# Kernel tuning notes

Hardware: AMD Instinct MI355X
Metric: run time of the kernel (lower is better)

## Reference

```python
import jax, jax.numpy as jnp
import numpy as np

B = 65536
FEAT = 64
NUM_CONT = 2
NUM_DISC = FEAT - NUM_CONT  # 62
D = 16                      # embedding_size
H1, H2 = 256, 128           # hidden_dims
DNN_IN = FEAT * D           # 1024


def setup_inputs() -> dict:
    key = jax.random.key(0)
    ks = jax.random.split(key, 12)
    # x: first NUM_DISC cols are binary category ids (stored as float), last NUM_CONT are 'continuous'
    x = jax.random.randint(ks[0], (B, FEAT), 0, 2).astype(jnp.float32)
    s = 0.05
    return {
        "x": x,
        # 62 embedding tables of shape (2, D), stacked: [NUM_DISC, 2, D]
        "emb_tables": jax.random.normal(ks[1], (NUM_DISC, 2, D), jnp.float32) * s,
        "Wc": jax.random.normal(ks[2], (NUM_CONT * D, NUM_CONT), jnp.float32) * s,  # cont_linear
        "bc": jnp.zeros((NUM_CONT * D,), jnp.float32),
        "Wf": jax.random.normal(ks[3], (1, FEAT), jnp.float32) * s,                 # fm_linear
        "bf": jnp.zeros((1,), jnp.float32),
        "W1": jax.random.normal(ks[4], (H1, DNN_IN), jnp.float32) * s,
        "b1": jnp.zeros((H1,), jnp.float32),
        "W2": jax.random.normal(ks[5], (H2, H1), jnp.float32) * s,
        "b2": jnp.zeros((H2,), jnp.float32),
    }


def reference(x, emb_tables, Wc, bc, Wf, bf, W1, b1, W2, b2):
    # --- embeddings ---
    disc_idx = x[:, :NUM_DISC].astype(jnp.int32)                     # [B, 62]
    # per-feature table gather: emb_tables[f, idx[b,f]] -> [B, 62, D]
    disc_embeds = emb_tables[jnp.arange(NUM_DISC)[None, :], disc_idx]
    cont = x[:, NUM_DISC:]                                           # [B, 2]
    cont_embeds = (cont @ Wc.T + bc).reshape(-1, NUM_CONT, D)        # [B, 2, D]
    all_embeds = jnp.concatenate([disc_embeds, cont_embeds], axis=1) # [B, 64, D]

    # --- FM first order ---
    fm_first = x @ Wf.T + bf                                         # [B, 1]

    # --- FM second order: sum_{i<j} <e_i, e_j> = 0.5 * ((sum_i e_i)^2 - sum_i e_i^2) summed over D
    sum_e = jnp.sum(all_embeds, axis=1)                              # [B, D]
    sum_sq = jnp.sum(all_embeds * all_embeds, axis=(1, 2))           # [B]
    fm_second = 0.5 * (jnp.sum(sum_e * sum_e, axis=1) - sum_sq)      # [B]
    fm_second = fm_second[:, None]                                   # [B, 1]

    # --- DNN ---
    h = all_embeds.reshape(x.shape[0], -1)                           # [B, 1024]
    h = jax.nn.relu(h @ W1.T + b1)                                   # [B, 256]
    h = jax.nn.relu(h @ W2.T + b2)                                   # [B, 128]

    return jnp.concatenate([fm_first + fm_second, h], axis=1)        # [B, 129]
```

## Files before the change

### kernel.cpp

```cpp
#include <hip/hip_runtime.h>
#include <hip/hip_bf16.h>


#define NROWS   65536
#define NFEAT   64
#define NDISC   62
#define DIM     16
#define K1      1024
#define H1N     256
#define H2N     128
#define OUTC    129

using f32x4  = __attribute__((ext_vector_type(4))) float;
using bf16x8 = __attribute__((ext_vector_type(8))) short;

__device__ __forceinline__ unsigned short f2bf(float f) {
    unsigned u = __builtin_bit_cast(unsigned, f);
    u = (u + 0x7FFFu + ((u >> 16) & 1u)) >> 16;
    return (unsigned short)u;
}

__device__ __forceinline__ void async16(const void* g, void* l) {
    __builtin_amdgcn_global_load_lds(
        (const __attribute__((address_space(1))) void*)g,
        (__attribute__((address_space(3))) void*)l, 16, 0, 0);
}

__global__ __launch_bounds__(256) void convert_w(const float* __restrict__ W1,
                                                 const float* __restrict__ W2,
                                                 unsigned short* __restrict__ W1b,
                                                 unsigned short* __restrict__ W2b) {
    int i = blockIdx.x * 256 + threadIdx.x;
    if (i < H1N * K1) W1b[i] = f2bf(W1[i]);
    if (i < H2N * H1N) W2b[i] = f2bf(W2[i]);
}

__global__ __launch_bounds__(256) void fm_kernel(const float* __restrict__ x,
                                                 const float* __restrict__ tbl,
                                                 const float* __restrict__ Wc,
                                                 const float* __restrict__ bc,
                                                 const float* __restrict__ Wf,
                                                 const float* __restrict__ bfp,
                                                 float* __restrict__ out) {
    __shared__ float tblL[NDISC * 2 * DIM];
    __shared__ float WcL[64];
    __shared__ float bcL[32];
    __shared__ float WfL[64];
    const int t = threadIdx.x, l = t & 63, w = t >> 6;
    const int d = l & 15;
    for (int i = t; i < NDISC * 2 * DIM; i += 256) tblL[i] = tbl[i];
    if (t < 64) WcL[t] = Wc[t];
    else if (t < 96) bcL[t - 64] = bc[t - 64];
    else if (t < 160) WfL[t - 96] = Wf[t - 96];
    __syncthreads();
    const float bf0 = bfp[0];

    const int waveId = blockIdx.x * 4 + w;
    #pragma unroll
    for (int it = 0; it < 2; ++it) {
        const int grp = waveId + it * 8192;
        const int row = grp * 4 + (l >> 4);
        const float4 v = *(const float4*)(x + (size_t)row * NFEAT + d * 4);

        unsigned long long m =
            ((unsigned long long)((int)v.x & 1)) |
            ((unsigned long long)((int)v.y & 1) << 1) |
            ((unsigned long long)((int)v.z & 1) << 2) |
            ((unsigned long long)((int)v.w & 1) << 3);
        m <<= (d * 4);
        m |= __shfl_xor(m, 1); m |= __shfl_xor(m, 2);
        m |= __shfl_xor(m, 4); m |= __shfl_xor(m, 8);
        const float c0 = __shfl(v.z, l | 15);
        const float c1 = __shfl(v.w, l | 15);

        float fp = v.x * WfL[4 * d] + v.y * WfL[4 * d + 1] +
                   v.z * WfL[4 * d + 2] + v.w * WfL[4 * d + 3];

        float se = 0.f, ssq = 0.f;
        #pragma unroll
        for (int f = 0; f < NDISC; ++f) {
            const int bit = (int)((m >> f) & 1ULL);
            const float e = tblL[(f * 2 + bit) * DIM + d];
            se += e; ssq += e * e;
        }
        {
            const float e62 = bcL[d]      + c0 * WcL[2 * d]        + c1 * WcL[2 * d + 1];
            const float e63 = bcL[16 + d] + c0 * WcL[2 * (16 + d)] + c1 * WcL[2 * (16 + d) + 1];
            se += e62 + e63; ssq += e62 * e62 + e63 * e63;
        }

        float u = se * se - ssq;
        u  += __shfl_xor(u, 1);  u  += __shfl_xor(u, 2);
        u  += __shfl_xor(u, 4);  u  += __shfl_xor(u, 8);
        fp += __shfl_xor(fp, 1); fp += __shfl_xor(fp, 2);
        fp += __shfl_xor(fp, 4); fp += __shfl_xor(fp, 8);
        if (d == 0) out[(size_t)row * OUTC] = fp + bf0 + 0.5f * u;
    }
}

__global__ __launch_bounds__(512, 4) void gemm_fused(
        const float* __restrict__ x,
        const float* __restrict__ tbl,
        const float* __restrict__ Wc,
        const float* __restrict__ bc,
        const unsigned short* __restrict__ W1b,
        const float* __restrict__ b1,
        const unsigned short* __restrict__ W2b,
        const float* __restrict__ b2,
        float* __restrict__ out) {
    __shared__ __align__(16) char smem[65536];
    unsigned short* ldsA  = (unsigned short*)(smem);
    unsigned short* ldsB  = (unsigned short*)(smem + 16384);
    unsigned char*  xb    = (unsigned char*)(smem + 49152);
    float*          contf = (float*)(smem + 57344);
    unsigned short* tblLb = (unsigned short*)(smem + 58368);
    float*          WcL   = (float*)(smem + 62336);
    float*          bcL   = (float*)(smem + 62592);
    unsigned short* H1t   = (unsigned short*)(smem);

    const int t  = threadIdx.x;
    const int l  = t & 63;
    const int w  = t >> 6;
    const int wr = w >> 2;
    const int wc = w & 3;
    const int m0 = blockIdx.x * 128;

    for (int i = t; i < NDISC * 2 * DIM; i += 512) tblLb[i] = f2bf(tbl[i]);
    if (t < 64) WcL[t] = Wc[t];
    if (t >= 64 && t < 96) bcL[t - 64] = bc[t - 64];

    {
        const int row = t >> 2, cbase = (t & 3) * 16;
        const float4* xp = (const float4*)(x + (size_t)(m0 + row) * NFEAT + cbase);
        #pragma unroll
        for (int q = 0; q < 4; ++q) {
            float4 v = xp[q];
            unsigned pk = ((unsigned)(int)v.x) | ((unsigned)(int)v.y << 8) |
                          ((unsigned)(int)v.z << 16) | ((unsigned)(int)v.w << 24);
            *(unsigned*)&xb[row * 64 + cbase + q * 4] = pk;
            if (cbase + q * 4 == 60) {
                contf[row * 2]     = v.z;
                contf[row * 2 + 1] = v.w;
            }
        }
    }
    __syncthreads();

    f32x4 acc[4][4] = {};

    for (int ks = 0; ks < 16; ++ks) {
        const int k0 = ks * 64;
        const int f0 = ks * 4;

        #pragma unroll
        for (int p = 0; p < 2; ++p) {
            const int chunk = p * 512 + t;
            const int row = chunk >> 3;
            const int cc  = chunk & 7;
            const int fl  = cc >> 1;
            const int d0  = (cc & 1) * 8;
            const int f   = f0 + fl;
            bf16x8 pk;
            if (f < NDISC) {
                const int bit = xb[row * 64 + f] & 1;
                pk = *(const bf16x8*)&tblLb[(f * 2 + bit) * DIM + d0];
            } else {
                const float c0v = contf[row * 2], c1v = contf[row * 2 + 1];
                const int j0 = (f - NDISC) * 16 + d0;
                #pragma unroll
                for (int dd = 0; dd < 8; ++dd) {
                    const int j = j0 + dd;
                    pk[dd] = (short)f2bf(bcL[j] + c0v * WcL[2 * j] + c1v * WcL[2 * j + 1]);
                }
            }
            *(bf16x8*)&ldsA[row * 64 + (cc ^ (row & 7)) * 8] = pk;
        }

        {
            unsigned short* dstbase = ldsB + w * 512;
            #pragma unroll
            for (int p = 0; p < 4; ++p) {
                const int chunk = p * 512 + t;
                const int row = chunk >> 3;
                const int cc  = chunk & 7;
                const int ccs = cc ^ (row & 7);
                async16(W1b + (size_t)row * K1 + k0 + ccs * 8, dstbase + p * 4096);
            }
        }
        __syncthreads();

        #pragma unroll
        for (int sub = 0; sub < 2; ++sub) {
            const int s = sub * 4 + (l >> 4);
            bf16x8 af[4], bfr[4];
            #pragma unroll
            for (int i = 0; i < 4; ++i) {
                const int ra = wr * 64 + i * 16 + (l & 15);
                af[i] = *(const bf16x8*)&ldsA[ra * 64 + (s ^ (ra & 7)) * 8];
            }
            #pragma unroll
            for (int j = 0; j < 4; ++j) {
                const int rb = wc * 64 + j * 16 + (l & 15);
                bfr[j] = *(const bf16x8*)&ldsB[rb * 64 + (s ^ (rb & 7)) * 8];
            }
            #pragma unroll
            for (int i = 0; i < 4; ++i)
                #pragma unroll
                for (int j = 0; j < 4; ++j)
                    acc[i][j] = __builtin_amdgcn_mfma_f32_16x16x32_bf16(af[i], bfr[j], acc[i][j], 0, 0, 0);
        }
        __syncthreads();
    }

    #pragma unroll
    for (int i = 0; i < 4; ++i) {
        const int rloc0 = wr * 64 + i * 16 + (l >> 4) * 4;
        #pragma unroll
        for (int j = 0; j < 4; ++j) {
            const int col  = wc * 64 + j * 16 + (l & 15);
            const int slot = col >> 3, cin = col & 7;
            const float bias = b1[col];
            #pragma unroll
            for (int r = 0; r < 4; ++r) {
                const int row = rloc0 + r;
                float v = acc[i][j][r] + bias;
                v = v > 0.f ? v : 0.f;
                H1t[row * 256 + (slot ^ (row & 7)) * 8 + cin] = f2bf(v);
            }
        }
    }
    __syncthreads();

    f32x4 acc2[4][2] = {};
    #pragma unroll
    for (int kk = 0; kk < 8; ++kk) {
        bf16x8 bfr2[2];
        #pragma unroll
        for (int j2 = 0; j2 < 2; ++j2) {
            const int nrow = wc * 32 + j2 * 16 + (l & 15);
            bfr2[j2] = *(const bf16x8*)(W2b + (size_t)nrow * H1N + kk * 32 + (l >> 4) * 8);
        }
        const int slot = kk * 4 + (l >> 4);
        #pragma unroll
        for (int i2 = 0; i2 < 4; ++i2) {
            const int ra = wr * 64 + i2 * 16 + (l & 15);
            const bf16x8 af2 = *(const bf16x8*)&H1t[ra * 256 + (slot ^ (ra & 7)) * 8];
            #pragma unroll
            for (int j2 = 0; j2 < 2; ++j2)
                acc2[i2][j2] = __builtin_amdgcn_mfma_f32_16x16x32_bf16(af2, bfr2[j2], acc2[i2][j2], 0, 0, 0);
        }
    }

    #pragma unroll
    for (int i2 = 0; i2 < 4; ++i2) {
        const int rbase = m0 + wr * 64 + i2 * 16 + (l >> 4) * 4;
        #pragma unroll
        for (int j2 = 0; j2 < 2; ++j2) {
            const int n = wc * 32 + j2 * 16 + (l & 15);
            const float bias = b2[n];
            #pragma unroll
            for (int r = 0; r < 4; ++r) {
                float v = acc2[i2][j2][r] + bias;
                v = v > 0.f ? v : 0.f;
                out[(size_t)(rbase + r) * OUTC + 1 + n] = v;
            }
        }
    }
}

extern "C" void kernel_launch(void* const* d_in, const int* in_sizes, int n_in,
                              void* d_out, int out_size, void* d_ws, size_t ws_size,
                              hipStream_t stream) {
    const float* x   = (const float*)d_in[0];
    const float* tbl = (const float*)d_in[1];
    const float* Wc  = (const float*)d_in[2];
    const float* bc  = (const float*)d_in[3];
    const float* Wf  = (const float*)d_in[4];
    const float* bfp = (const float*)d_in[5];
    const float* W1  = (const float*)d_in[6];
    const float* b1  = (const float*)d_in[7];
    const float* W2  = (const float*)d_in[8];
    const float* b2  = (const float*)d_in[9];
    float* out = (float*)d_out;

    char* ws = (char*)d_ws;
    unsigned short* W1b = (unsigned short*)ws;
    unsigned short* W2b = (unsigned short*)(ws + 524288);

    convert_w<<<dim3(H1N * K1 / 256), dim3(256), 0, stream>>>(W1, W2, W1b, W2b);
    fm_kernel<<<dim3(2048), dim3(256), 0, stream>>>(x, tbl, Wc, bc, Wf, bfp, out);
    gemm_fused<<<dim3(NROWS / 128), dim3(512), 0, stream>>>(x, tbl, Wc, bc, W1b, b1,
                                                            W2b, b2, out);
}
```

Before: 140.3 us.

## Fold embedding tables into W1 to shrink first GEMM from K=1024 to K=64

Since each discrete feature takes a binary value and the continuous embeddings are linear in x, the first DNN layer is rewritten as x @ Dp^T + biasTot. A prep kernel precomputes Dp, the 256x64 per-feature weight delta, and the folded bias from the tables, Wc, bc, W1 and b1. The main GEMM then does a single K=64 step on x converted to bf16 instead of sixteen K-steps over gathered embeddings, which removes most MFMA work and the W1 streaming. The cost is a small extra prep launch, plus bf16 rounding of the folded weights, which changes numerics slightly. The precomputation depends only on the weights and is redone on every call.

```diff
diff --git a/kernel.cpp b/kernel.cpp
--- a/kernel.cpp
+++ b/kernel.cpp
@@ -26,13 +26,48 @@
         (__attribute__((address_space(3))) void*)l, 16, 0, 0);
 }
 
-__global__ __launch_bounds__(256) void convert_w(const float* __restrict__ W1,
-                                                 const float* __restrict__ W2,
-                                                 unsigned short* __restrict__ W1b,
-                                                 unsigned short* __restrict__ W2b) {
+__global__ __launch_bounds__(256) void convert_w2(const float* __restrict__ W2,
+                                                  unsigned short* __restrict__ W2b) {
     int i = blockIdx.x * 256 + threadIdx.x;
-    if (i < H1N * K1) W1b[i] = f2bf(W1[i]);
     if (i < H2N * H1N) W2b[i] = f2bf(W2[i]);
+}
+
+__global__ __launch_bounds__(256) void prep(const float* __restrict__ tbl,
+                                            const float* __restrict__ Wc,
+                                            const float* __restrict__ bc,
+                                            const float* __restrict__ W1,
+                                            const float* __restrict__ b1,
+                                            unsigned short* __restrict__ Dp,
+                                            float* __restrict__ biasTot) {
+    const int g = blockIdx.x * 256 + threadIdx.x;
+    const int c = g >> 6, k = g & 63;
+    const float* w1r = W1 + (size_t)c * K1;
+    float delta = 0.f, part = 0.f;
+    if (k < NDISC) {
+        #pragma unroll
+        for (int d = 0; d < 16; ++d) {
+            const float t0 = tbl[(k * 2) * 16 + d];
+            const float t1 = tbl[(k * 2 + 1) * 16 + d];
+            const float w  = w1r[k * 16 + d];
+            delta += (t1 - t0) * w;
+            part  += t0 * w;
+        }
+    } else if (k == 62) {
+        #pragma unroll
+        for (int j = 0; j < 32; ++j) delta += Wc[j * 2] * w1r[992 + j];
+        #pragma unroll
+        for (int j = 0; j < 16; ++j) part += bc[j] * w1r[992 + j];
+    } else {
+        #pragma unroll
+        for (int j = 0; j < 32; ++j) delta += Wc[j * 2 + 1] * w1r[992 + j];
+        #pragma unroll
+        for (int j = 0; j < 16; ++j) part += bc[16 + j] * w1r[1008 + j];
+    }
+    Dp[(size_t)c * 64 + k] = f2bf(delta);
+    part += __shfl_xor(part, 1);  part += __shfl_xor(part, 2);
+    part += __shfl_xor(part, 4);  part += __shfl_xor(part, 8);
+    part += __shfl_xor(part, 16); part += __shfl_xor(part, 32);
+    if (k == 0) biasTot[c] = part + b1[c];
 }
 
 __global__ __launch_bounds__(256) void fm_kernel(const float* __restrict__ x,
@@ -100,23 +135,15 @@
 
 __global__ __launch_bounds__(512, 4) void gemm_fused(
         const float* __restrict__ x,
-        const float* __restrict__ tbl,
-        const float* __restrict__ Wc,
-        const float* __restrict__ bc,
-        const unsigned short* __restrict__ W1b,
-        const float* __restrict__ b1,
+        const unsigned short* __restrict__ Dp,
+        const float* __restrict__ biasTot,
         const unsigned short* __restrict__ W2b,
         const float* __restrict__ b2,
         float* __restrict__ out) {
     __shared__ __align__(16) char smem[65536];
-    unsigned short* ldsA  = (unsigned short*)(smem);
-    unsigned short* ldsB  = (unsigned short*)(smem + 16384);
-    unsigned char*  xb    = (unsigned char*)(smem + 49152);
-    float*          contf = (float*)(smem + 57344);
-    unsigned short* tblLb = (unsigned short*)(smem + 58368);
-    float*          WcL   = (float*)(smem + 62336);
-    float*          bcL   = (float*)(smem + 62592);
-    unsigned short* H1t   = (unsigned short*)(smem);
+    unsigned short* ldsA = (unsigned short*)(smem);
+    unsigned short* ldsB = (unsigned short*)(smem + 16384);
+    unsigned short* H1t  = (unsigned short*)(smem);
 
     const int t  = threadIdx.x;
     const int l  = t & 63;
@@ -125,92 +152,57 @@
     const int wc = w & 3;
     const int m0 = blockIdx.x * 128;
 
-    for (int i = t; i < NDISC * 2 * DIM; i += 512) tblLb[i] = f2bf(tbl[i]);
-    if (t < 64) WcL[t] = Wc[t];
-    if (t >= 64 && t < 96) bcL[t - 64] = bc[t - 64];
-
     {
-        const int row = t >> 2, cbase = (t & 3) * 16;
-        const float4* xp = (const float4*)(x + (size_t)(m0 + row) * NFEAT + cbase);
-        #pragma unroll
-        for (int q = 0; q < 4; ++q) {
-            float4 v = xp[q];
-            unsigned pk = ((unsigned)(int)v.x) | ((unsigned)(int)v.y << 8) |
-                          ((unsigned)(int)v.z << 16) | ((unsigned)(int)v.w << 24);
-            *(unsigned*)&xb[row * 64 + cbase + q * 4] = pk;
-            if (cbase + q * 4 == 60) {
-                contf[row * 2]     = v.z;
-                contf[row * 2 + 1] = v.w;
-            }
-        }
-    }
-    __syncthreads();
-
-    f32x4 acc[4][4] = {};
-
-    for (int ks = 0; ks < 16; ++ks) {
-        const int k0 = ks * 64;
-        const int f0 = ks * 4;
-
-        #pragma unroll
-        for (int p = 0; p < 2; ++p) {
+        unsigned short* dstbase = ldsB + w * 512;
+        #pragma unroll
+        for (int p = 0; p < 4; ++p) {
             const int chunk = p * 512 + t;
             const int row = chunk >> 3;
             const int cc  = chunk & 7;
-            const int fl  = cc >> 1;
-            const int d0  = (cc & 1) * 8;
-            const int f   = f0 + fl;
+            const int ccs = cc ^ (row & 7);
+            async16(Dp + (size_t)row * 64 + ccs * 8, dstbase + p * 4096);
+        }
+    }
+
+    {
+        const int row = t >> 2, q3 = t & 3;
+        const float4* xp = (const float4*)(x + (size_t)(m0 + row) * NFEAT + q3 * 16);
+        #pragma unroll
+        for (int qq = 0; qq < 2; ++qq) {
+            float4 v0 = xp[qq * 2], v1 = xp[qq * 2 + 1];
             bf16x8 pk;
-            if (f < NDISC) {
-                const int bit = xb[row * 64 + f] & 1;
-                pk = *(const bf16x8*)&tblLb[(f * 2 + bit) * DIM + d0];
-            } else {
-                const float c0v = contf[row * 2], c1v = contf[row * 2 + 1];
-                const int j0 = (f - NDISC) * 16 + d0;
-                #pragma unroll
-                for (int dd = 0; dd < 8; ++dd) {
-                    const int j = j0 + dd;
-                    pk[dd] = (short)f2bf(bcL[j] + c0v * WcL[2 * j] + c1v * WcL[2 * j + 1]);
-                }
-            }
+            pk[0] = (short)f2bf(v0.x); pk[1] = (short)f2bf(v0.y);
+            pk[2] = (short)f2bf(v0.z); pk[3] = (short)f2bf(v0.w);
+            pk[4] = (short)f2bf(v1.x); pk[5] = (short)f2bf(v1.y);
+            pk[6] = (short)f2bf(v1.z); pk[7] = (short)f2bf(v1.w);
+            const int cc = q3 * 2 + qq;
             *(bf16x8*)&ldsA[row * 64 + (cc ^ (row & 7)) * 8] = pk;
         }
-
-        {
-            unsigned short* dstbase = ldsB + w * 512;
-            #pragma unroll
-            for (int p = 0; p < 4; ++p) {
-                const int chunk = p * 512 + t;
-                const int row = chunk >> 3;
-                const int cc  = chunk & 7;
-                const int ccs = cc ^ (row & 7);
-                async16(W1b + (size_t)row * K1 + k0 + ccs * 8, dstbase + p * 4096);
-            }
-        }
-        __syncthreads();
-
-        #pragma unroll
-        for (int sub = 0; sub < 2; ++sub) {
-            const int s = sub * 4 + (l >> 4);
-            bf16x8 af[4], bfr[4];
-            #pragma unroll
-            for (int i = 0; i < 4; ++i) {
-                const int ra = wr * 64 + i * 16 + (l & 15);
-                af[i] = *(const bf16x8*)&ldsA[ra * 64 + (s ^ (ra & 7)) * 8];
-            }
-            #pragma unroll
-            for (int j = 0; j < 4; ++j) {
-                const int rb = wc * 64 + j * 16 + (l & 15);
-                bfr[j] = *(const bf16x8*)&ldsB[rb * 64 + (s ^ (rb & 7)) * 8];
-            }
-            #pragma unroll
-            for (int i = 0; i < 4; ++i)
-                #pragma unroll
-                for (int j = 0; j < 4; ++j)
-                    acc[i][j] = __builtin_amdgcn_mfma_f32_16x16x32_bf16(af[i], bfr[j], acc[i][j], 0, 0, 0);
-        }
-        __syncthreads();
-    }
+    }
+    __syncthreads();
+
+    f32x4 acc[4][4] = {};
+    #pragma unroll
+    for (int sub = 0; sub < 2; ++sub) {
+        const int s = sub * 4 + (l >> 4);
+        bf16x8 af[4], bfr[4];
+        #pragma unroll
+        for (int i = 0; i < 4; ++i) {
+            const int ra = wr * 64 + i * 16 + (l & 15);
+            af[i] = *(const bf16x8*)&ldsA[ra * 64 + (s ^ (ra & 7)) * 8];
+        }
+        #pragma unroll
+        for (int j = 0; j < 4; ++j) {
+            const int rb = wc * 64 + j * 16 + (l & 15);
+            bfr[j] = *(const bf16x8*)&ldsB[rb * 64 + (s ^ (rb & 7)) * 8];
+        }
+        #pragma unroll
+        for (int i = 0; i < 4; ++i)
+            #pragma unroll
+            for (int j = 0; j < 4; ++j)
+                acc[i][j] = __builtin_amdgcn_mfma_f32_16x16x32_bf16(af[i], bfr[j], acc[i][j], 0, 0, 0);
+    }
+    __syncthreads();
 
     #pragma unroll
     for (int i = 0; i < 4; ++i) {
@@ -219,7 +211,7 @@
         for (int j = 0; j < 4; ++j) {
             const int col  = wc * 64 + j * 16 + (l & 15);
             const int slot = col >> 3, cin = col & 7;
-            const float bias = b1[col];
+            const float bias = biasTot[col];
             #pragma unroll
             for (int r = 0; r < 4; ++r) {
                 const int row = rloc0 + r;
@@ -284,11 +276,12 @@
     float* out = (float*)d_out;
 
     char* ws = (char*)d_ws;
-    unsigned short* W1b = (unsigned short*)ws;
-    unsigned short* W2b = (unsigned short*)(ws + 524288);
-
-    convert_w<<<dim3(H1N * K1 / 256), dim3(256), 0, stream>>>(W1, W2, W1b, W2b);
+    unsigned short* W2b     = (unsigned short*)ws;
+    unsigned short* Dp      = (unsigned short*)(ws + 65536);
+    float*          biasTot = (float*)(ws + 98304);
+
+    convert_w2<<<dim3(H2N * H1N / 256), dim3(256), 0, stream>>>(W2, W2b);
+    prep<<<dim3(64), dim3(256), 0, stream>>>(tbl, Wc, bc, W1, b1, Dp, biasTot);
     fm_kernel<<<dim3(2048), dim3(256), 0, stream>>>(x, tbl, Wc, bc, Wf, bfp, out);
-    gemm_fused<<<dim3(NROWS / 128), dim3(512), 0, stream>>>(x, tbl, Wc, bc, W1b, b1,
-                                                            W2b, b2, out);
-}
+    gemm_fused<<<dim3(NROWS / 128), dim3(512), 0, stream>>>(x, Dp, biasTot, W2b, b2, out);
+}
```

Result: faster. 118.6 us (-15.5%).
